# Kernel optimization log

Hardware: AMD Instinct MI355X
Metric: run time of the kernel (lower is better)

Reference implementation:

```python
import jax, jax.numpy as jnp
import numpy as np

HEADS = 2
DIM_HEAD = 64


def _wn_linear(x, v, g, b):
    # torch weight_norm: W = g * v / ||v|| (norm over input dim, per output row)
    W = v * (g / jnp.linalg.norm(v, axis=1))[:, None]
    return x @ W.T + b


def setup_inputs() -> dict:
    key = jax.random.key(0)
    ks = jax.random.split(key, 8)
    b, n, dim = 2, 4096, 128
    inner = HEADS * DIM_HEAD  # 128
    hidden = dim              # FeedForward(inner_dim, dim)
    s = 0.05
    return {
        "x": jax.random.normal(ks[0], (b, n, dim), dtype=jnp.float32),
        "v_qkv": jax.random.normal(ks[1], (3 * inner, dim), dtype=jnp.float32) * s,
        "g_qkv": jnp.ones((3 * inner,), jnp.float32),
        "b_qkv": jnp.zeros((3 * inner,), jnp.float32),
        "v_ff1": jax.random.normal(ks[2], (hidden, inner), dtype=jnp.float32) * s,
        "g_ff1": jnp.ones((hidden,), jnp.float32),
        "b_ff1": jnp.zeros((hidden,), jnp.float32),
        "v_ff2": jax.random.normal(ks[3], (inner, hidden), dtype=jnp.float32) * s,
        "g_ff2": jnp.ones((inner,), jnp.float32),
        "b_ff2": jnp.zeros((inner,), jnp.float32),
    }


def reference(x, v_qkv, g_qkv, b_qkv, v_ff1, g_ff1, b_ff1, v_ff2, g_ff2, b_ff2):
    b, n, d = x.shape
    scale = DIM_HEAD ** (-0.5)

    # ---- spectral mask: exp(-cdist(x,x)/(2*mean(cdist)^2)), shape [b,n,n]
    sq = jnp.sum(x * x, axis=-1)  # [b,n]
    d2 = sq[:, :, None] + sq[:, None, :] - 2.0 * jnp.einsum('bnd,bmd->bnm', x, x)
    spe_dist = jnp.sqrt(jnp.maximum(d2, 0.0))
    sigma_spe = jnp.mean(spe_dist)
    spe = jnp.exp(-spe_dist / (2.0 * sigma_spe ** 2))

    # ---- spatial mask: pairwise grid distances on sqrt(n) x sqrt(n) grid, [n,n]
    hw = int(round(n ** 0.5))
    gx, gy = jnp.meshgrid(jnp.arange(hw), jnp.arange(hw), indexing='ij')
    grid = jnp.stack((gx, gy), axis=-1).astype(jnp.float32).reshape(n, 2)
    diff = grid[:, None, :] - grid[None, :, :]
    spa_dist = jnp.sqrt(jnp.sum(diff ** 2, axis=-1))
    sigma_spa = jnp.mean(spa_dist)
    spa = jnp.exp(-spa_dist / (2.0 * sigma_spa ** 2))  # same for every b, h

    # ---- qkv projection (weight-normed linear)
    qkv = _wn_linear(x, v_qkv, g_qkv, b_qkv)  # [b,n,3*inner]
    q, k, v = jnp.split(qkv, 3, axis=-1)
    split_heads = lambda t: t.reshape(b, n, HEADS, DIM_HEAD).transpose(0, 2, 1, 3)
    q, k, v = split_heads(q), split_heads(k), split_heads(v)  # [b,h,n,dh]

    dots = jnp.einsum('bhid,bhjd->bhij', q, k) * scale
    dots = dots * spe[:, None, :, :] * spa[None, None, :, :]
    attn = jax.nn.softmax(dots, axis=-1)  # dropout is identity at inference
    out = jnp.einsum('bhij,bhjd->bhid', attn, v)
    out = out.transpose(0, 2, 1, 3).reshape(b, n, HEADS * DIM_HEAD)

    # ---- to_out FeedForward: wn-Linear -> GELU -> wn-Linear (dropout = id)
    h1 = jax.nn.gelu(_wn_linear(out, v_ff1, g_ff1, b_ff1), approximate=False)
    return _wn_linear(h1, v_ff2, g_ff2, b_ff2)
```

## Files before the change

kernel.cpp:

```cpp
#include <hip/hip_runtime.h>
#include <hip/hip_fp16.h>
#include <math.h>

typedef unsigned short u16;
typedef _Float16 f16x8 __attribute__((ext_vector_type(8)));
typedef float f32x4 __attribute__((ext_vector_type(4)));

#define LOG2E 1.4426950408889634f

static __device__ __forceinline__ u16 f2h(float f) {
    _Float16 h = (_Float16)f;
    return __builtin_bit_cast(u16, h);
}
static __device__ __forceinline__ float h2f(u16 u) {
    return (float)__builtin_bit_cast(_Float16, u);
}

__global__ __launch_bounds__(256) void prep_x(const float* __restrict__ x,
                                              u16* __restrict__ xh,
                                              float* __restrict__ sq) {
    int wave = threadIdx.x >> 6, lane = threadIdx.x & 63;
    int row = blockIdx.x * 4 + wave;
    const float2 v = *reinterpret_cast<const float2*>(x + (size_t)row * 128 + lane * 2);
    float ss = v.x * v.x + v.y * v.y;
#pragma unroll
    for (int m = 1; m < 64; m <<= 1) ss += __shfl_xor(ss, m, 64);
    unsigned int packed = (unsigned int)f2h(v.x) | ((unsigned int)f2h(v.y) << 16);
    *reinterpret_cast<unsigned int*>(xh + (size_t)row * 128 + lane * 2) = packed;
    if (lane == 0) sq[row] = ss;
}

__global__ __launch_bounds__(64) void prep_w(const float* __restrict__ vq, const float* __restrict__ gq,
                                             const float* __restrict__ v1, const float* __restrict__ g1,
                                             const float* __restrict__ v2, const float* __restrict__ g2,
                                             u16* __restrict__ wq, u16* __restrict__ w1, u16* __restrict__ w2) {
    int row = blockIdx.x, lane = threadIdx.x;
    const float* src; float gv; u16* dst; int r;
    if (row < 384)      { r = row;       src = vq + (size_t)r * 128; gv = gq[r]; dst = wq + (size_t)r * 128; }
    else if (row < 512) { r = row - 384; src = v1 + (size_t)r * 128; gv = g1[r]; dst = w1 + (size_t)r * 128; }
    else                { r = row - 512; src = v2 + (size_t)r * 128; gv = g2[r]; dst = w2 + (size_t)r * 128; }
    float2 v = *reinterpret_cast<const float2*>(src + lane * 2);
    float ss = v.x * v.x + v.y * v.y;
#pragma unroll
    for (int m = 1; m < 64; m <<= 1) ss += __shfl_xor(ss, m, 64);
    float sc = gv / sqrtf(ss);
    unsigned int packed = (unsigned int)f2h(v.x * sc) | ((unsigned int)f2h(v.y * sc) << 16);
    *reinterpret_cast<unsigned int*>(dst + lane * 2) = packed;
}

__global__ __launch_bounds__(256) void sigma_gemm(const u16* __restrict__ xh,
                                                  const float* __restrict__ sq,
                                                  float* __restrict__ partial) {
    __shared__ u16 xi[128][136];
    __shared__ u16 xj[128][136];
    int bid = blockIdx.x;
    int b = bid >> 10, rest = bid & 1023;
    int i0 = (rest >> 5) * 128, j0 = (rest & 31) * 128;
    int tid = threadIdx.x;
    const u16* xsrc = xh + (size_t)b * 4096 * 128;
    for (int t = tid; t < 2048; t += 256) {
        int row = t >> 4, c = (t & 15) * 8;
        *reinterpret_cast<uint4*>(&xi[row][c]) =
            *reinterpret_cast<const uint4*>(xsrc + (size_t)(i0 + row) * 128 + c);
    }
    for (int t = tid; t < 2048; t += 256) {
        int row = t >> 4, c = (t & 15) * 8;
        *reinterpret_cast<uint4*>(&xj[row][c]) =
            *reinterpret_cast<const uint4*>(xsrc + (size_t)(j0 + row) * 128 + c);
    }
    __syncthreads();
    int wave = tid >> 6, lane = tid & 63, lr = lane & 15, lg = lane >> 4;
    f16x8 ai[2][4];
#pragma unroll
    for (int m2 = 0; m2 < 2; ++m2)
#pragma unroll
        for (int ks = 0; ks < 4; ++ks)
            ai[m2][ks] = *reinterpret_cast<const f16x8*>(&xi[wave * 32 + m2 * 16 + lr][ks * 32 + lg * 8]);
    const float* sqb = sq + (size_t)b * 4096;
    float sqi[2][4];
#pragma unroll
    for (int m2 = 0; m2 < 2; ++m2)
#pragma unroll
        for (int r = 0; r < 4; ++r)
            sqi[m2][r] = sqb[i0 + wave * 32 + m2 * 16 + lg * 4 + r];
    float lsum = 0.f;
#pragma unroll
    for (int c = 0; c < 8; ++c) {
        f16x8 bj[4];
#pragma unroll
        for (int ks = 0; ks < 4; ++ks)
            bj[ks] = *reinterpret_cast<const f16x8*>(&xj[c * 16 + lr][ks * 32 + lg * 8]);
        float sqj = sqb[j0 + c * 16 + lr];
#pragma unroll
        for (int m2 = 0; m2 < 2; ++m2) {
            f32x4 acc = {0.f, 0.f, 0.f, 0.f};
#pragma unroll
            for (int ks = 0; ks < 4; ++ks)
                acc = __builtin_amdgcn_mfma_f32_16x16x32_f16(ai[m2][ks], bj[ks], acc, 0, 0, 0);
#pragma unroll
            for (int r = 0; r < 4; ++r) {
                float d2 = fmaf(-2.f, acc[r], sqi[m2][r] + sqj);
                lsum += sqrtf(fmaxf(d2, 0.f));
            }
        }
    }
#pragma unroll
    for (int m = 1; m < 64; m <<= 1) lsum += __shfl_xor(lsum, m, 64);
    if (lane == 0) atomicAdd(&partial[bid], lsum);
}

__global__ __launch_bounds__(256) void sigma_fin(const float* __restrict__ partial,
                                                 float* __restrict__ accum) {
    __shared__ float red[4];
    float s = 0.f;
    for (int i = threadIdx.x; i < 2048; i += 256) s += partial[i];
#pragma unroll
    for (int m = 1; m < 64; m <<= 1) s += __shfl_xor(s, m, 64);
    int w = threadIdx.x >> 6;
    if ((threadIdx.x & 63) == 0) red[w] = s;
    __syncthreads();
    if (threadIdx.x == 0) {
        float sigma = (red[0] + red[1] + red[2] + red[3]) / 33554432.f;
        accum[1] = LOG2E / (2.f * sigma * sigma);
    }
}

__global__ __launch_bounds__(256) void qkv_gemm(const u16* __restrict__ xh, const u16* __restrict__ wq,
                                                const float* __restrict__ bq,
                                                u16* __restrict__ q_ws, u16* __restrict__ k_ws,
                                                u16* __restrict__ vt_ws) {
    int cg = blockIdx.x & 1;
    int tok0 = (blockIdx.x >> 1) * 64 + (threadIdx.x >> 6) * 16;
    int lane = threadIdx.x & 63, lr = lane & 15, lg = lane >> 4;
    f16x8 a[4];
#pragma unroll
    for (int ks = 0; ks < 4; ++ks)
        a[ks] = *reinterpret_cast<const f16x8*>(xh + (size_t)(tok0 + lr) * 128 + ks * 32 + lg * 8);
#pragma unroll
    for (int ci = 0; ci < 12; ++ci) {
        int c = cg * 12 + ci;
        f32x4 acc = {0.f, 0.f, 0.f, 0.f};
#pragma unroll
        for (int ks = 0; ks < 4; ++ks) {
            f16x8 bw = *reinterpret_cast<const f16x8*>(wq + (size_t)(c * 16 + lr) * 128 + ks * 32 + lg * 8);
            acc = __builtin_amdgcn_mfma_f32_16x16x32_f16(a[ks], bw, acc, 0, 0, 0);
        }
        int j = c * 16 + lr;
        float bias = bq[j];
        float sc = (j < 128) ? 0.125f : 1.0f;
#pragma unroll
        for (int r = 0; r < 4; ++r) {
            int tokg = tok0 + lg * 4 + r;
            int b = tokg >> 12, n = tokg & 4095;
            u16 hv = f2h((acc[r] + bias) * sc);
            if (j < 128) {
                q_ws[((size_t)(b * 2 + (j >> 6)) * 4096 + n) * 64 + (j & 63)] = hv;
            } else if (j < 256) {
                int jj = j - 128;
                k_ws[((size_t)(b * 2 + (jj >> 6)) * 4096 + n) * 64 + (jj & 63)] = hv;
            } else {
                int jj = j - 256;
                vt_ws[((size_t)(b * 2 + (jj >> 6)) * 64 + (jj & 63)) * 4096 + n] = hv;
            }
        }
    }
}

__global__ __launch_bounds__(256, 2) void attn_fused(
    const u16* __restrict__ xh, const float* __restrict__ sq,
    const u16* __restrict__ q_ws, const u16* __restrict__ k_ws, const u16* __restrict__ vt_ws,
    const float* __restrict__ accum, u16* __restrict__ opart, float* __restrict__ l_ws,
    float c2L) {
    __shared__ u16 k_lds[2][64][72];
    __shared__ u16 vt_lds[2][64][72];
    __shared__ u16 xk_lds[64][136];
    __shared__ u16 p_lds[4][2][16][72];
    __shared__ float sq_lds[64];

    const float c1L = accum[1];
    const float NEG8L = -8.0f * LOG2E;
    int idx = blockIdx.x;
    int qt = idx & 63, split = (idx >> 6) & 3, b = idx >> 8;
    int tid = threadIdx.x;
    int w = tid >> 6, lane = tid & 63, lr = lane & 15, lg = lane >> 4;
    int q0 = qt * 64 + w * 16;

    f16x8 aq[2][2], axq[4];
#pragma unroll
    for (int h = 0; h < 2; ++h)
#pragma unroll
        for (int ks = 0; ks < 2; ++ks)
            aq[h][ks] = *reinterpret_cast<const f16x8*>(
                q_ws + ((size_t)(b * 2 + h) * 4096 + q0 + lr) * 64 + ks * 32 + lg * 8);
#pragma unroll
    for (int ks = 0; ks < 4; ++ks)
        axq[ks] = *reinterpret_cast<const f16x8*>(
            xh + ((size_t)b * 4096 + q0 + lr) * 128 + ks * 32 + lg * 8);

    float sqi[4], ixf[4], iyf[4];
#pragma unroll
    for (int r = 0; r < 4; ++r) {
        int i = q0 + lg * 4 + r;
        sqi[r] = sq[(size_t)b * 4096 + i];
        ixf[r] = (float)(i >> 6);
        iyf[r] = (float)(i & 63);
    }

    const f32x4 zero4 = {0.f, 0.f, 0.f, 0.f};
    f32x4 O[2][4];
    float lsum[2][4];
#pragma unroll
    for (int h = 0; h < 2; ++h)
#pragma unroll
        for (int vd = 0; vd < 4; ++vd) O[h][vd] = zero4;
#pragma unroll
    for (int h = 0; h < 2; ++h)
#pragma unroll
        for (int r = 0; r < 4; ++r) lsum[h][r] = 0.f;

    for (int t = 0; t < 16; ++t) {
        int kb = split * 1024 + t * 64;
#pragma unroll
        for (int it = 0; it < 4; ++it) {
            int i2 = tid + it * 256;
            int h2 = i2 >> 9, rem = i2 & 511;
            int row = rem >> 3, c8 = rem & 7;
            *reinterpret_cast<uint4*>(&k_lds[h2][row][c8 * 8]) =
                *reinterpret_cast<const uint4*>(k_ws + ((size_t)(b * 2 + h2) * 4096 + kb + row) * 64 + c8 * 8);
        }
#pragma unroll
        for (int it = 0; it < 4; ++it) {
            int i2 = tid + it * 256;
            int h2 = i2 >> 9, rem = i2 & 511;
            int row = rem >> 3, c8 = rem & 7;
            *reinterpret_cast<uint4*>(&vt_lds[h2][row][c8 * 8]) =
                *reinterpret_cast<const uint4*>(vt_ws + ((size_t)(b * 2 + h2) * 64 + row) * 4096 + kb + c8 * 8);
        }
#pragma unroll
        for (int it = 0; it < 4; ++it) {
            int i2 = tid + it * 256;
            int row = i2 >> 4, c16 = i2 & 15;
            *reinterpret_cast<uint4*>(&xk_lds[row][c16 * 8]) =
                *reinterpret_cast<const uint4*>(xh + ((size_t)b * 4096 + kb + row) * 128 + c16 * 8);
        }
        if (tid < 64) sq_lds[tid] = sq[(size_t)b * 4096 + kb + tid];
        __syncthreads();

#pragma unroll
        for (int c = 0; c < 4; ++c) {
            f32x4 Dacc = zero4, S0 = zero4, S1 = zero4;
#pragma unroll
            for (int ks = 0; ks < 4; ++ks) {
                f16x8 bx = *reinterpret_cast<const f16x8*>(&xk_lds[c * 16 + lr][ks * 32 + lg * 8]);
                Dacc = __builtin_amdgcn_mfma_f32_16x16x32_f16(axq[ks], bx, Dacc, 0, 0, 0);
            }
#pragma unroll
            for (int ks = 0; ks < 2; ++ks) {
                f16x8 bk0 = *reinterpret_cast<const f16x8*>(&k_lds[0][c * 16 + lr][ks * 32 + lg * 8]);
                S0 = __builtin_amdgcn_mfma_f32_16x16x32_f16(aq[0][ks], bk0, S0, 0, 0, 0);
                f16x8 bk1 = *reinterpret_cast<const f16x8*>(&k_lds[1][c * 16 + lr][ks * 32 + lg * 8]);
                S1 = __builtin_amdgcn_mfma_f32_16x16x32_f16(aq[1][ks], bk1, S1, 0, 0, 0);
            }
            int j = kb + c * 16 + lr;
            float sqj = sq_lds[c * 16 + lr];
            float jxf = (float)(j >> 6), jyf = (float)(j & 63);
#pragma unroll
            for (int r = 0; r < 4; ++r) {
                float d2 = fmaf(-2.f, Dacc[r], sqi[r] + sqj);
                float sd = sqrtf(fmaxf(d2, 0.f));
                float dx = ixf[r] - jxf, dy = iyf[r] - jyf;
                float spad = sqrtf(fmaf(dx, dx, dy * dy));
                float tt = fmaf(sd, c1L, spad * c2L);
                float msk = exp2f(-tt);
                float p0 = exp2f(fmaf(S0[r] * msk, LOG2E, NEG8L));
                float p1 = exp2f(fmaf(S1[r] * msk, LOG2E, NEG8L));
                p0 = fminf(p0, 60000.f);
                p1 = fminf(p1, 60000.f);
                lsum[0][r] += p0;
                lsum[1][r] += p1;
                p_lds[w][0][lg * 4 + r][c * 16 + lr] = f2h(p0);
                p_lds[w][1][lg * 4 + r][c * 16 + lr] = f2h(p1);
            }
        }
#pragma unroll
        for (int h = 0; h < 2; ++h)
#pragma unroll
            for (int ks = 0; ks < 2; ++ks) {
                f16x8 pa = *reinterpret_cast<const f16x8*>(&p_lds[w][h][lr][ks * 32 + lg * 8]);
#pragma unroll
                for (int vd = 0; vd < 4; ++vd) {
                    f16x8 bv = *reinterpret_cast<const f16x8*>(&vt_lds[h][vd * 16 + lr][ks * 32 + lg * 8]);
                    O[h][vd] = __builtin_amdgcn_mfma_f32_16x16x32_f16(pa, bv, O[h][vd], 0, 0, 0);
                }
            }
        __syncthreads();
    }
#pragma unroll
    for (int r = 0; r < 4; ++r) {
        int q = q0 + lg * 4 + r;
#pragma unroll
        for (int h = 0; h < 2; ++h) {
            float ls = lsum[h][r];
#pragma unroll
            for (int m = 1; m < 16; m <<= 1) ls += __shfl_xor(ls, m, 64);
            size_t base = (((size_t)split * 2 + b) * 2 + h) * 4096 + q;
            if (lr == 0) l_ws[base] = ls;
#pragma unroll
            for (int vd = 0; vd < 4; ++vd)
                opart[base * 64 + vd * 16 + lr] = f2h(O[h][vd][r]);
        }
    }
}

__global__ __launch_bounds__(256) void combine(const u16* __restrict__ opart,
                                               const float* __restrict__ l_ws,
                                               u16* __restrict__ attn_h) {
    int e = blockIdx.x * 256 + threadIdx.x;
    int tok = e >> 7, d = e & 127;
    int b = tok >> 12, n = tok & 4095;
    int h = d >> 6, dh = d & 63;
    float O = 0.f, L = 0.f;
#pragma unroll
    for (int s = 0; s < 4; ++s) {
        size_t base = (((size_t)s * 2 + b) * 2 + h) * 4096 + n;
        O += h2f(opart[base * 64 + dh]);
        L += l_ws[base];
    }
    attn_h[(size_t)tok * 128 + d] = f2h(O / L);
}

__global__ __launch_bounds__(256) void ff_gemm(const u16* __restrict__ in, const u16* __restrict__ w,
                                               const float* __restrict__ bias, void* __restrict__ out,
                                               int act) {
    int cg = blockIdx.x & 1;
    int tok0 = (blockIdx.x >> 1) * 64 + (threadIdx.x >> 6) * 16;
    int lane = threadIdx.x & 63, lr = lane & 15, lg = lane >> 4;
    f16x8 a[4];
#pragma unroll
    for (int ks = 0; ks < 4; ++ks)
        a[ks] = *reinterpret_cast<const f16x8*>(in + (size_t)(tok0 + lr) * 128 + ks * 32 + lg * 8);
#pragma unroll
    for (int ci = 0; ci < 4; ++ci) {
        int c = cg * 4 + ci;
        f32x4 acc = {0.f, 0.f, 0.f, 0.f};
#pragma unroll
        for (int ks = 0; ks < 4; ++ks) {
            f16x8 bw = *reinterpret_cast<const f16x8*>(w + (size_t)(c * 16 + lr) * 128 + ks * 32 + lg * 8);
            acc = __builtin_amdgcn_mfma_f32_16x16x32_f16(a[ks], bw, acc, 0, 0, 0);
        }
        int j = c * 16 + lr;
        float bv = bias[j];
#pragma unroll
        for (int r = 0; r < 4; ++r) {
            int tok = tok0 + lg * 4 + r;
            float val = acc[r] + bv;
            if (act) {
                float g = 0.5f * val * (1.f + erff(val * 0.7071067811865475f));
                ((u16*)out)[(size_t)tok * 128 + j] = f2h(g);
            } else {
                ((float*)out)[(size_t)tok * 128 + j] = val;
            }
        }
    }
}

extern "C" void kernel_launch(void* const* d_in, const int* in_sizes, int n_in,
                              void* d_out, int out_size, void* d_ws, size_t ws_size,
                              hipStream_t stream) {
    const float* x     = (const float*)d_in[0];
    const float* v_qkv = (const float*)d_in[1];
    const float* g_qkv = (const float*)d_in[2];
    const float* b_qkv = (const float*)d_in[3];
    const float* v_ff1 = (const float*)d_in[4];
    const float* g_ff1 = (const float*)d_in[5];
    const float* b_ff1 = (const float*)d_in[6];
    const float* v_ff2 = (const float*)d_in[7];
    const float* g_ff2 = (const float*)d_in[8];
    const float* b_ff2 = (const float*)d_in[9];

    char* w = (char*)d_ws;
    size_t off = 0;
    float* accum   = (float*)(w + off); off += 256;
    float* partial = (float*)(w + off); off += 2048 * 4;
    u16* xh      = (u16*)(w + off);   off += (size_t)8192 * 128 * 2;
    float* sqv   = (float*)(w + off); off += (size_t)8192 * 4;
    u16* wqkv    = (u16*)(w + off);   off += (size_t)384 * 128 * 2;
    u16* w1      = (u16*)(w + off);   off += (size_t)128 * 128 * 2;
    u16* w2      = (u16*)(w + off);   off += (size_t)128 * 128 * 2;
    u16* q_ws    = (u16*)(w + off);   off += (size_t)4 * 4096 * 64 * 2;
    u16* k_ws    = (u16*)(w + off);   off += (size_t)4 * 4096 * 64 * 2;
    u16* vt_ws   = (u16*)(w + off);   off += (size_t)4 * 4096 * 64 * 2;
    u16* opart   = (u16*)(w + off);   off += (size_t)16 * 4096 * 64 * 2;
    float* l_ws  = (float*)(w + off); off += (size_t)16 * 4096 * 4;
    u16* attn_h  = (u16*)(w + off);   off += (size_t)8192 * 128 * 2;
    u16* h1      = (u16*)(w + off);   off += (size_t)8192 * 128 * 2;

    double ssum = 0.0;
    for (int dx = -63; dx <= 63; ++dx) {
        int adx = dx < 0 ? -dx : dx;
        for (int dy = -63; dy <= 63; ++dy) {
            int ady = dy < 0 ? -dy : dy;
            ssum += (double)(64 - adx) * (double)(64 - ady) * sqrt((double)(dx * dx + dy * dy));
        }
    }
    float sigma_spa = (float)(ssum / (4096.0 * 4096.0));
    float c2L = LOG2E / (2.0f * sigma_spa * sigma_spa);

    hipMemsetAsync(w, 0, 256 + 2048 * 4, stream);

    prep_x<<<2048, 256, 0, stream>>>(x, xh, sqv);
    prep_w<<<640, 64, 0, stream>>>(v_qkv, g_qkv, v_ff1, g_ff1, v_ff2, g_ff2, wqkv, w1, w2);
    sigma_gemm<<<2048, 256, 0, stream>>>(xh, sqv, partial);
    sigma_fin<<<1, 256, 0, stream>>>(partial, accum);
    qkv_gemm<<<256, 256, 0, stream>>>(xh, wqkv, b_qkv, q_ws, k_ws, vt_ws);
    attn_fused<<<512, 256, 0, stream>>>(xh, sqv, q_ws, k_ws, vt_ws, accum, opart, l_ws, c2L);
    combine<<<4096, 256, 0, stream>>>(opart, l_ws, attn_h);
    ff_gemm<<<256, 256, 0, stream>>>(attn_h, w1, b_ff1, (void*)h1, 1);
    ff_gemm<<<256, 256, 0, stream>>>(h1, w2, b_ff2, d_out, 0);
}
```

Measured before the change: 235.4 us.

## Precompute spatial mask table, use raw sqrt/exp, split attention keys eight ways

Adds a kernel that precomputes the spatial Gaussian mask as a 127x4096 lookup table indexed by row offset, so the attention inner loop loads it instead of computing a sqrt and an exp per element. Replaces sqrtf/exp2f with raw v_sqrt_f32/v_exp_f32 instructions and drops the fp16 overflow clamp. Halves the key tile to 32 and doubles the key-split count to 8, giving 1024 blocks with smaller LDS and an occupancy hint of 4. The cost is more partial outputs for the combine step, extra table memory traffic, and possible accuracy or overflow risk from the raw intrinsics and the removed clamp.

```diff
diff --git a/kernel.cpp b/kernel.cpp
--- a/kernel.cpp
+++ b/kernel.cpp
@@ -14,6 +14,12 @@
 }
 static __device__ __forceinline__ float h2f(u16 u) {
     return (float)__builtin_bit_cast(_Float16, u);
+}
+static __device__ __forceinline__ float fsqrt_raw(float x) {
+    float r; asm("v_sqrt_f32 %0, %1" : "=v"(r) : "v"(x)); return r;
+}
+static __device__ __forceinline__ float fexp2_raw(float x) {
+    float r; asm("v_exp_f32 %0, %1" : "=v"(r) : "v"(x)); return r;
 }
 
 __global__ __launch_bounds__(256) void prep_x(const float* __restrict__ x,
@@ -46,6 +52,15 @@
     float sc = gv / sqrtf(ss);
     unsigned int packed = (unsigned int)f2h(v.x * sc) | ((unsigned int)f2h(v.y * sc) << 16);
     *reinterpret_cast<unsigned int*>(dst + lane * 2) = packed;
+}
+
+__global__ __launch_bounds__(256) void spa_tab_k(float* __restrict__ tab, float c2) {
+    int id = blockIdx.x * 256 + threadIdx.x;
+    int dxi = id >> 12, rem = id & 4095;
+    int iy = rem >> 6, jy = rem & 63;
+    float dx = (float)(dxi - 63), dy = (float)(iy - jy);
+    float d = fsqrt_raw(fmaf(dx, dx, dy * dy));
+    tab[id] = LOG2E * fexp2_raw(-d * c2 * LOG2E);
 }
 
 __global__ __launch_bounds__(256) void sigma_gemm(const u16* __restrict__ xh,
@@ -100,7 +115,7 @@
 #pragma unroll
             for (int r = 0; r < 4; ++r) {
                 float d2 = fmaf(-2.f, acc[r], sqi[m2][r] + sqj);
-                lsum += sqrtf(fmaxf(d2, 0.f));
+                lsum += fsqrt_raw(fmaxf(d2, 0.f));
             }
         }
     }
@@ -121,7 +136,7 @@
     __syncthreads();
     if (threadIdx.x == 0) {
         float sigma = (red[0] + red[1] + red[2] + red[3]) / 33554432.f;
-        accum[1] = LOG2E / (2.f * sigma * sigma);
+        accum[1] = -LOG2E / (2.f * sigma * sigma);
     }
 }
 
@@ -166,21 +181,21 @@
     }
 }
 
-__global__ __launch_bounds__(256, 2) void attn_fused(
+__global__ __launch_bounds__(256, 4) void attn_fused(
     const u16* __restrict__ xh, const float* __restrict__ sq,
     const u16* __restrict__ q_ws, const u16* __restrict__ k_ws, const u16* __restrict__ vt_ws,
-    const float* __restrict__ accum, u16* __restrict__ opart, float* __restrict__ l_ws,
-    float c2L) {
-    __shared__ u16 k_lds[2][64][72];
-    __shared__ u16 vt_lds[2][64][72];
-    __shared__ u16 xk_lds[64][136];
-    __shared__ u16 p_lds[4][2][16][72];
-    __shared__ float sq_lds[64];
-
-    const float c1L = accum[1];
+    const float* __restrict__ accum, const float* __restrict__ spa,
+    u16* __restrict__ opart, float* __restrict__ l_ws) {
+    __shared__ u16 k_lds[2][32][72];
+    __shared__ u16 vt_lds[2][64][40];
+    __shared__ u16 xk_lds[32][136];
+    __shared__ u16 p_lds[4][2][16][40];
+    __shared__ float sq_lds[32];
+
+    const float nc1L = accum[1];
     const float NEG8L = -8.0f * LOG2E;
     int idx = blockIdx.x;
-    int qt = idx & 63, split = (idx >> 6) & 3, b = idx >> 8;
+    int qt = idx & 63, split = (idx >> 6) & 7, b = idx >> 9;
     int tid = threadIdx.x;
     int w = tid >> 6, lane = tid & 63, lr = lane & 15, lg = lane >> 4;
     int q0 = qt * 64 + w * 16;
@@ -197,13 +212,12 @@
         axq[ks] = *reinterpret_cast<const f16x8*>(
             xh + ((size_t)b * 4096 + q0 + lr) * 128 + ks * 32 + lg * 8);
 
-    float sqi[4], ixf[4], iyf[4];
+    float sqi[4];
+    int rowoff[4];
 #pragma unroll
     for (int r = 0; r < 4; ++r) {
-        int i = q0 + lg * 4 + r;
-        sqi[r] = sq[(size_t)b * 4096 + i];
-        ixf[r] = (float)(i >> 6);
-        iyf[r] = (float)(i & 63);
+        sqi[r] = sq[(size_t)b * 4096 + q0 + lg * 4 + r];
+        rowoff[r] = (w * 16 + lg * 4 + r) * 64 + lr;
     }
 
     const f32x4 zero4 = {0.f, 0.f, 0.f, 0.f};
@@ -219,35 +233,37 @@
         for (int r = 0; r < 4; ++r) lsum[h][r] = 0.f;
 
     for (int t = 0; t < 16; ++t) {
-        int kb = split * 1024 + t * 64;
-#pragma unroll
-        for (int it = 0; it < 4; ++it) {
+        int kb = split * 512 + t * 32;
+        int dxi = qt - (kb >> 6) + 63;
+        const float* spa_t = spa + (size_t)dxi * 4096 + (kb & 63);
+#pragma unroll
+        for (int it = 0; it < 2; ++it) {
             int i2 = tid + it * 256;
-            int h2 = i2 >> 9, rem = i2 & 511;
+            int h2 = i2 >> 8, rem = i2 & 255;
             int row = rem >> 3, c8 = rem & 7;
             *reinterpret_cast<uint4*>(&k_lds[h2][row][c8 * 8]) =
                 *reinterpret_cast<const uint4*>(k_ws + ((size_t)(b * 2 + h2) * 4096 + kb + row) * 64 + c8 * 8);
         }
 #pragma unroll
-        for (int it = 0; it < 4; ++it) {
+        for (int it = 0; it < 2; ++it) {
             int i2 = tid + it * 256;
-            int h2 = i2 >> 9, rem = i2 & 511;
-            int row = rem >> 3, c8 = rem & 7;
-            *reinterpret_cast<uint4*>(&vt_lds[h2][row][c8 * 8]) =
-                *reinterpret_cast<const uint4*>(vt_ws + ((size_t)(b * 2 + h2) * 64 + row) * 4096 + kb + c8 * 8);
-        }
-#pragma unroll
-        for (int it = 0; it < 4; ++it) {
+            int h2 = i2 >> 8, rem = i2 & 255;
+            int row = rem >> 2, c4 = rem & 3;
+            *reinterpret_cast<uint4*>(&vt_lds[h2][row][c4 * 8]) =
+                *reinterpret_cast<const uint4*>(vt_ws + ((size_t)(b * 2 + h2) * 64 + row) * 4096 + kb + c4 * 8);
+        }
+#pragma unroll
+        for (int it = 0; it < 2; ++it) {
             int i2 = tid + it * 256;
             int row = i2 >> 4, c16 = i2 & 15;
             *reinterpret_cast<uint4*>(&xk_lds[row][c16 * 8]) =
                 *reinterpret_cast<const uint4*>(xh + ((size_t)b * 4096 + kb + row) * 128 + c16 * 8);
         }
-        if (tid < 64) sq_lds[tid] = sq[(size_t)b * 4096 + kb + tid];
+        if (tid < 32) sq_lds[tid] = sq[(size_t)b * 4096 + kb + tid];
         __syncthreads();
 
 #pragma unroll
-        for (int c = 0; c < 4; ++c) {
+        for (int c = 0; c < 2; ++c) {
             f32x4 Dacc = zero4, S0 = zero4, S1 = zero4;
 #pragma unroll
             for (int ks = 0; ks < 4; ++ks) {
@@ -261,21 +277,18 @@
                 f16x8 bk1 = *reinterpret_cast<const f16x8*>(&k_lds[1][c * 16 + lr][ks * 32 + lg * 8]);
                 S1 = __builtin_amdgcn_mfma_f32_16x16x32_f16(aq[1][ks], bk1, S1, 0, 0, 0);
             }
-            int j = kb + c * 16 + lr;
             float sqj = sq_lds[c * 16 + lr];
-            float jxf = (float)(j >> 6), jyf = (float)(j & 63);
+            float sp[4];
+#pragma unroll
+            for (int r = 0; r < 4; ++r) sp[r] = spa_t[rowoff[r] + c * 16];
 #pragma unroll
             for (int r = 0; r < 4; ++r) {
                 float d2 = fmaf(-2.f, Dacc[r], sqi[r] + sqj);
-                float sd = sqrtf(fmaxf(d2, 0.f));
-                float dx = ixf[r] - jxf, dy = iyf[r] - jyf;
-                float spad = sqrtf(fmaf(dx, dx, dy * dy));
-                float tt = fmaf(sd, c1L, spad * c2L);
-                float msk = exp2f(-tt);
-                float p0 = exp2f(fmaf(S0[r] * msk, LOG2E, NEG8L));
-                float p1 = exp2f(fmaf(S1[r] * msk, LOG2E, NEG8L));
-                p0 = fminf(p0, 60000.f);
-                p1 = fminf(p1, 60000.f);
+                float sd = fsqrt_raw(fmaxf(d2, 0.f));
+                float spe = fexp2_raw(sd * nc1L);
+                float mskL = sp[r] * spe;
+                float p0 = fexp2_raw(fmaf(S0[r], mskL, NEG8L));
+                float p1 = fexp2_raw(fmaf(S1[r], mskL, NEG8L));
                 lsum[0][r] += p0;
                 lsum[1][r] += p1;
                 p_lds[w][0][lg * 4 + r][c * 16 + lr] = f2h(p0);
@@ -283,16 +296,14 @@
             }
         }
 #pragma unroll
-        for (int h = 0; h < 2; ++h)
-#pragma unroll
-            for (int ks = 0; ks < 2; ++ks) {
-                f16x8 pa = *reinterpret_cast<const f16x8*>(&p_lds[w][h][lr][ks * 32 + lg * 8]);
-#pragma unroll
-                for (int vd = 0; vd < 4; ++vd) {
-                    f16x8 bv = *reinterpret_cast<const f16x8*>(&vt_lds[h][vd * 16 + lr][ks * 32 + lg * 8]);
-                    O[h][vd] = __builtin_amdgcn_mfma_f32_16x16x32_f16(pa, bv, O[h][vd], 0, 0, 0);
-                }
-            }
+        for (int h = 0; h < 2; ++h) {
+            f16x8 pa = *reinterpret_cast<const f16x8*>(&p_lds[w][h][lr][lg * 8]);
+#pragma unroll
+            for (int vd = 0; vd < 4; ++vd) {
+                f16x8 bv = *reinterpret_cast<const f16x8*>(&vt_lds[h][vd * 16 + lr][lg * 8]);
+                O[h][vd] = __builtin_amdgcn_mfma_f32_16x16x32_f16(pa, bv, O[h][vd], 0, 0, 0);
+            }
+        }
         __syncthreads();
     }
 #pragma unroll
@@ -321,7 +332,7 @@
     int h = d >> 6, dh = d & 63;
     float O = 0.f, L = 0.f;
 #pragma unroll
-    for (int s = 0; s < 4; ++s) {
+    for (int s = 0; s < 8; ++s) {
         size_t base = (((size_t)s * 2 + b) * 2 + h) * 4096 + n;
         O += h2f(opart[base * 64 + dh]);
         L += l_ws[base];
@@ -382,6 +393,7 @@
     size_t off = 0;
     float* accum   = (float*)(w + off); off += 256;
     float* partial = (float*)(w + off); off += 2048 * 4;
+    float* spa_tab = (float*)(w + off); off += (size_t)127 * 4096 * 4;
     u16* xh      = (u16*)(w + off);   off += (size_t)8192 * 128 * 2;
     float* sqv   = (float*)(w + off); off += (size_t)8192 * 4;
     u16* wqkv    = (u16*)(w + off);   off += (size_t)384 * 128 * 2;
@@ -390,8 +402,8 @@
     u16* q_ws    = (u16*)(w + off);   off += (size_t)4 * 4096 * 64 * 2;
     u16* k_ws    = (u16*)(w + off);   off += (size_t)4 * 4096 * 64 * 2;
     u16* vt_ws   = (u16*)(w + off);   off += (size_t)4 * 4096 * 64 * 2;
-    u16* opart   = (u16*)(w + off);   off += (size_t)16 * 4096 * 64 * 2;
-    float* l_ws  = (float*)(w + off); off += (size_t)16 * 4096 * 4;
+    u16* opart   = (u16*)(w + off);   off += (size_t)32 * 4096 * 64 * 2;
+    float* l_ws  = (float*)(w + off); off += (size_t)32 * 4096 * 4;
     u16* attn_h  = (u16*)(w + off);   off += (size_t)8192 * 128 * 2;
     u16* h1      = (u16*)(w + off);   off += (size_t)8192 * 128 * 2;
 
@@ -404,16 +416,17 @@
         }
     }
     float sigma_spa = (float)(ssum / (4096.0 * 4096.0));
-    float c2L = LOG2E / (2.0f * sigma_spa * sigma_spa);
+    float c2 = 1.0f / (2.0f * sigma_spa * sigma_spa);
 
     hipMemsetAsync(w, 0, 256 + 2048 * 4, stream);
 
     prep_x<<<2048, 256, 0, stream>>>(x, xh, sqv);
     prep_w<<<640, 64, 0, stream>>>(v_qkv, g_qkv, v_ff1, g_ff1, v_ff2, g_ff2, wqkv, w1, w2);
+    spa_tab_k<<<2032, 256, 0, stream>>>(spa_tab, c2);
     sigma_gemm<<<2048, 256, 0, stream>>>(xh, sqv, partial);
     sigma_fin<<<1, 256, 0, stream>>>(partial, accum);
     qkv_gemm<<<256, 256, 0, stream>>>(xh, wqkv, b_qkv, q_ws, k_ws, vt_ws);
-    attn_fused<<<512, 256, 0, stream>>>(xh, sqv, q_ws, k_ws, vt_ws, accum, opart, l_ws, c2L);
+    attn_fused<<<1024, 256, 0, stream>>>(xh, sqv, q_ws, k_ws, vt_ws, accum, spa_tab, opart, l_ws);
     combine<<<4096, 256, 0, stream>>>(opart, l_ws, attn_h);
     ff_gemm<<<256, 256, 0, stream>>>(attn_h, w1, b_ff1, (void*)h1, 1);
     ff_gemm<<<256, 256, 0, stream>>>(h1, w2, b_ff2, d_out, 0);
```

Result: faster. 212.2 us (-9.8%).
